# Kernel optimization log

Hardware: AMD Instinct MI355X
Metric: run time of the kernel (lower is better)

## Reference

```python
import jax, jax.numpy as jnp
import numpy as np

B, S, E, D = 4, 2048, 1024, 1024
NEG_INF = float('-inf')


def setup_inputs() -> dict:
    key = jax.random.key(0)
    ks = jax.random.split(key, 10)
    query = jax.random.normal(ks[0], (B, S, E), dtype=jnp.float32)
    key_t = jax.random.normal(ks[1], (B, S, E), dtype=jnp.float32)
    value = jax.random.normal(ks[2], (B, S, E), dtype=jnp.float32)
    # Linear params (torch convention: y = x @ W.T + b)
    sc = 1.0 / np.sqrt(E)
    Wq = jax.random.uniform(ks[3], (D, E), jnp.float32, -sc, sc)
    bq = jax.random.uniform(ks[4], (D,), jnp.float32, -sc, sc)
    Wk = jax.random.uniform(ks[5], (D, E), jnp.float32, -sc, sc)
    bk = jax.random.uniform(ks[6], (D,), jnp.float32, -sc, sc)
    Wv = jax.random.uniform(ks[7], (D, E), jnp.float32, -sc, sc)
    bv = jax.random.uniform(ks[8], (D,), jnp.float32, -sc, sc)
    # padding mask: True = masked key position; ensure key 0 is never masked
    # so no row is fully -inf under the causal mask.
    lengths = jax.random.randint(ks[9], (B, 1, 1), 1, S + 1)  # valid length per batch
    pos = jnp.arange(S)[None, None, :]
    padding_mask = pos >= lengths  # [B,1,S] bool
    return {
        "query": query, "key": key_t, "value": value,
        "Wq": Wq, "bq": bq, "Wk": Wk, "bk": bk, "Wv": Wv, "bv": bv,
        "padding_mask": padding_mask, "look_ahead_mask": 1,
    }


def reference(query, key, value, Wq, bq, Wk, bk, Wv, bv, padding_mask, look_ahead_mask):
    q = query @ Wq.T + bq          # [B,S,D]
    k = key @ Wk.T + bk            # [B,S,D]
    v = value @ Wv.T + bv          # [B,S,D]
    scale = jnp.sqrt(jnp.asarray(q.shape[-1], q.dtype))
    qk = jnp.einsum('bqd,bkd->bqk', q, k) / scale  # [B,S,S]
    if padding_mask is not None:
        qk = jnp.where(padding_mask, NEG_INF, qk)
    if look_ahead_mask:
        causal = jnp.where(
            jnp.tril(jnp.ones((q.shape[1], k.shape[1]), dtype=bool)),
            jnp.asarray(0.0, qk.dtype), jnp.asarray(NEG_INF, qk.dtype))
        qk = qk + causal
    attn = jax.nn.softmax(qk, axis=-1)
    return jnp.einsum('bqk,bkd->bqd', attn, v)  # [B,S,D]
```

## Files before the change

kernel.cpp:

```cpp
#include <hip/hip_runtime.h>
#include <cstdint>
#include <cstddef>

#define B_ 4
#define S_ 2048
#define E_ 1024
#define D_ 1024
#define MFLAT (B_*S_)

typedef __attribute__((ext_vector_type(4))) float f32x4;
typedef __attribute__((ext_vector_type(8))) short short8;
typedef unsigned short u16;
typedef unsigned int   u32;

__device__ __forceinline__ u16 f2bf(float f) {
  u32 u = __float_as_uint(f);
  u = (u + 0x7fffu + ((u >> 16) & 1u)) >> 16;
  return (u16)u;
}

__device__ __forceinline__ void gll16(const void* g, void* lds) {
  __builtin_amdgcn_global_load_lds(
      (const __attribute__((address_space(1))) void*)g,
      (__attribute__((address_space(3))) void*)lds, 16, 0, 0);
}

__device__ __forceinline__ void gemm_core(
    const u16* __restrict__ Ag, int lda,
    const u16* __restrict__ Bg, int ldb,
    int ksteps, u16* As, u16* Bs, f32x4 acc[4][4])
{
  const int tid = threadIdx.x;
  const int w = tid >> 6;
  const int l = tid & 63;
  const int srow = l >> 2;
  const int skb  = (l & 3) << 3;
  const int fr = l & 15;
  const int fk = (l >> 4) << 3;
  const int wr = (w >> 1) << 6;
  const int wc = (w & 1) << 6;
  const int c0 = w * 2, c1 = c0 + 1;

  const u16* a0 = Ag + (size_t)(c0*16 + srow)*lda + skb;
  const u16* a1 = Ag + (size_t)(c1*16 + srow)*lda + skb;
  const u16* b0 = Bg + (size_t)(c0*16 + srow)*ldb + skb;
  const u16* b1 = Bg + (size_t)(c1*16 + srow)*ldb + skb;

  for (int kt = 0; kt < ksteps; ++kt) {
    gll16(a0, As + c0*512);
    gll16(a1, As + c1*512);
    gll16(b0, Bs + c0*512);
    gll16(b1, Bs + c1*512);
    a0 += 32; a1 += 32; b0 += 32; b1 += 32;
    __syncthreads();
    short8 af[4], bfr[4];
#pragma unroll
    for (int i = 0; i < 4; ++i)
      af[i] = *(const short8*)(As + ((wr + i*16 + fr) << 5) + fk);
#pragma unroll
    for (int j = 0; j < 4; ++j)
      bfr[j] = *(const short8*)(Bs + ((wc + j*16 + fr) << 5) + fk);
#pragma unroll
    for (int i = 0; i < 4; ++i)
#pragma unroll
      for (int j = 0; j < 4; ++j)
        acc[i][j] = __builtin_amdgcn_mfma_f32_16x16x32_bf16(af[i], bfr[j], acc[i][j], 0, 0, 0);
    __syncthreads();
  }
}

__global__ __launch_bounds__(256) void cvt_kernel(const float* __restrict__ src,
                                                  u16* __restrict__ dst, int n4) {
  int idx = blockIdx.x * blockDim.x + threadIdx.x;
  int stride = gridDim.x * blockDim.x;
  for (int i = idx; i < n4; i += stride) {
    float4 f = ((const float4*)src)[i];
    ushort4 o;
    o.x = f2bf(f.x); o.y = f2bf(f.y); o.z = f2bf(f.z); o.w = f2bf(f.w);
    ((ushort4*)dst)[i] = o;
  }
}

__global__ __launch_bounds__(256) void lengths_kernel(const void* __restrict__ mask,
                                                      int* __restrict__ lengths) {
  __shared__ int isbytes;
  const int t = threadIdx.x;
  if (t == 0) isbytes = 0;
  __syncthreads();
  const int* wi = (const int*)mask;
  int bad = 0;
  for (int idx = t; idx < (B_*S_)/4; idx += 256) {
    int v = wi[idx];
    if (v != 0 && v != 1) bad = 1;
  }
  if (bad) atomicOr(&isbytes, 1);
  __syncthreads();
  const int isb = isbytes;
  const int w = t >> 6, l = t & 63;
  const unsigned char* mb = (const unsigned char*)mask;
  int cnt = 0;
  for (int j = l; j < S_; j += 64) {
    int val = isb ? (int)mb[(size_t)w*S_ + j] : wi[(size_t)w*S_ + j];
    cnt += (val == 0);
  }
#pragma unroll
  for (int off = 32; off >= 1; off >>= 1) cnt += __shfl_xor(cnt, off);
  if (l == 0) lengths[w] = cnt;
}

__global__ __launch_bounds__(256) void proj_kernel(
    const u16* __restrict__ X, const u16* __restrict__ W,
    const float* __restrict__ bq, const float* __restrict__ bk, const float* __restrict__ bv,
    u16* __restrict__ q, u16* __restrict__ k, u16* __restrict__ v)
{
  __shared__ u16 As[4096], Bs[4096];
  const int nt = blockIdx.x, mt = blockIdx.y, z = blockIdx.z;
  const u16* Xz = X + (size_t)z * ((size_t)MFLAT * E_);
  const u16* Wz = W + (size_t)z * ((size_t)D_ * E_);
  f32x4 acc[4][4];
#pragma unroll
  for (int i = 0; i < 4; ++i)
#pragma unroll
    for (int j = 0; j < 4; ++j) acc[i][j] = (f32x4){0.f,0.f,0.f,0.f};
  gemm_core(Xz + (size_t)(mt*128)*E_, E_, Wz + (size_t)(nt*128)*E_, E_, E_/32, As, Bs, acc);

  const float* bias = (z == 0) ? bq : (z == 1) ? bk : bv;
  u16* out = (z == 0) ? q : (z == 1) ? k : v;
  const int tid = threadIdx.x, w = tid >> 6, l = tid & 63;
  const int wr = (w >> 1) << 6, wc = (w & 1) << 6;
  const int orow = mt*128 + wr + ((l >> 4) << 2);
  const int ocol = nt*128 + wc + (l & 15);
#pragma unroll
  for (int i = 0; i < 4; ++i)
#pragma unroll
    for (int j = 0; j < 4; ++j) {
      const int col = ocol + j*16;
      const float bcol = bias[col];
#pragma unroll
      for (int r = 0; r < 4; ++r) {
        const int row = orow + i*16 + r;
        out[(size_t)row*D_ + col] = f2bf(acc[i][j][r] + bcol);
      }
    }
}

__global__ __launch_bounds__(256) void transpose_kernel(
    const u16* __restrict__ v, u16* __restrict__ vT)
{
  __shared__ u16 tl[64][68];
  const int xt = blockIdx.x;
  const int yt = blockIdx.y;
  const int b  = blockIdx.z;
  const int t = threadIdx.x;
  const int r0 = t >> 4;
  const int c4 = (t & 15) << 2;
  const u16* src = v + ((size_t)b*S_ + yt*64)*D_ + xt*64;
#pragma unroll
  for (int rr = r0; rr < 64; rr += 16) {
    ushort4 u = *(const ushort4*)(src + (size_t)rr*D_ + c4);
    tl[rr][c4+0] = u.x; tl[rr][c4+1] = u.y; tl[rr][c4+2] = u.z; tl[rr][c4+3] = u.w;
  }
  __syncthreads();
  u16* dst = vT + ((size_t)b*D_ + xt*64)*S_ + yt*64;
#pragma unroll
  for (int rr = r0; rr < 64; rr += 16) {
    ushort4 u;
    u.x = tl[c4+0][rr]; u.y = tl[c4+1][rr]; u.z = tl[c4+2][rr]; u.w = tl[c4+3][rr];
    *(ushort4*)(dst + (size_t)rr*S_ + c4) = u;
  }
}

__global__ __launch_bounds__(256) void qk_kernel(
    const u16* __restrict__ q, const u16* __restrict__ k,
    const int* __restrict__ lengths, float* __restrict__ scores)
{
  const int tx = blockIdx.x, ty = blockIdx.y, b = blockIdx.z;
  if (tx > ty) return;
  const int len = lengths[b];
  if (tx * 128 >= len) return;
  __shared__ u16 As[4096], Bs[4096];
  f32x4 acc[4][4];
#pragma unroll
  for (int i = 0; i < 4; ++i)
#pragma unroll
    for (int j = 0; j < 4; ++j) acc[i][j] = (f32x4){0.f,0.f,0.f,0.f};
  const u16* Aq = q + ((size_t)b*S_ + (size_t)ty*128) * D_;
  const u16* Bk = k + ((size_t)b*S_ + (size_t)tx*128) * D_;
  gemm_core(Aq, D_, Bk, D_, D_/32, As, Bs, acc);

  const int tid = threadIdx.x, w = tid >> 6, l = tid & 63;
  const int wr = (w >> 1) << 6, wc = (w & 1) << 6;
  const int orow = ty*128 + wr + ((l >> 4) << 2);
  const int ocol = tx*128 + wc + (l & 15);
  float* sb = scores + (size_t)b*S_*S_;
#pragma unroll
  for (int i = 0; i < 4; ++i)
#pragma unroll
    for (int j = 0; j < 4; ++j)
#pragma unroll
      for (int r = 0; r < 4; ++r)
        sb[(size_t)(orow + i*16 + r)*S_ + (ocol + j*16)] = acc[i][j][r] * 0.03125f;
}

__global__ __launch_bounds__(256) void softmax_kernel(
    const float* __restrict__ scores, const int* __restrict__ lengths,
    u16* __restrict__ P)
{
  const int i = blockIdx.x, b = blockIdx.y;
  const int len = lengths[b];
  const int kmax = min(i + 1, len);
  const float* row = scores + ((size_t)b*S_ + i)*S_;
  u16* prow = P + ((size_t)b*S_ + i)*S_;
  const int t = threadIdx.x;
  const int j0 = t * 8;
  float v[8];
  {
    float4 x0 = *(const float4*)(row + j0);
    float4 x1 = *(const float4*)(row + j0 + 4);
    v[0]=x0.x; v[1]=x0.y; v[2]=x0.z; v[3]=x0.w;
    v[4]=x1.x; v[5]=x1.y; v[6]=x1.z; v[7]=x1.w;
  }
  float m = -3.4e38f;
#pragma unroll
  for (int e = 0; e < 8; ++e) if (j0 + e < kmax) m = fmaxf(m, v[e]);
#pragma unroll
  for (int off = 32; off >= 1; off >>= 1) m = fmaxf(m, __shfl_xor(m, off));
  __shared__ float redm[4], reds[4];
  if ((t & 63) == 0) redm[t >> 6] = m;
  __syncthreads();
  m = fmaxf(fmaxf(redm[0], redm[1]), fmaxf(redm[2], redm[3]));
  float s = 0.f, ex[8];
#pragma unroll
  for (int e = 0; e < 8; ++e) {
    ex[e] = (j0 + e < kmax) ? __expf(v[e] - m) : 0.f;
    s += ex[e];
  }
#pragma unroll
  for (int off = 32; off >= 1; off >>= 1) s += __shfl_xor(s, off);
  if ((t & 63) == 0) reds[t >> 6] = s;
  __syncthreads();
  s = reds[0] + reds[1] + reds[2] + reds[3];
  const float inv = 1.0f / s;
  short8 o;
#pragma unroll
  for (int e = 0; e < 8; ++e) o[e] = (short)f2bf(ex[e] * inv);
  *(short8*)(prow + j0) = o;
}

__global__ __launch_bounds__(256) void pv_kernel(
    const u16* __restrict__ P, const u16* __restrict__ vT,
    const int* __restrict__ lengths, float* __restrict__ out)
{
  const int xt = blockIdx.x, ty = blockIdx.y, b = blockIdx.z;
  const int len = lengths[b];
  const int kend = min(ty*128 + 128, len);
  const int ksteps = (kend + 31) >> 5;
  __shared__ u16 As[4096], Bs[4096];
  f32x4 acc[4][4];
#pragma unroll
  for (int i = 0; i < 4; ++i)
#pragma unroll
    for (int j = 0; j < 4; ++j) acc[i][j] = (f32x4){0.f,0.f,0.f,0.f};
  const u16* Ap = P  + ((size_t)b*S_ + (size_t)ty*128)*S_;
  const u16* Bv = vT + ((size_t)b*D_ + (size_t)xt*128)*S_;
  gemm_core(Ap, S_, Bv, S_, ksteps, As, Bs, acc);

  const int tid = threadIdx.x, w = tid >> 6, l = tid & 63;
  const int wr = (w >> 1) << 6, wc = (w & 1) << 6;
  const int orow = ty*128 + wr + ((l >> 4) << 2);
  const int ocol = xt*128 + wc + (l & 15);
  float* ob = out + (size_t)b*S_*D_;
#pragma unroll
  for (int i = 0; i < 4; ++i)
#pragma unroll
    for (int j = 0; j < 4; ++j)
#pragma unroll
      for (int r = 0; r < 4; ++r)
        ob[(size_t)(orow + i*16 + r)*D_ + (ocol + j*16)] = acc[i][j][r];
}

extern "C" void kernel_launch(void* const* d_in, const int* in_sizes, int n_in,
                              void* d_out, int out_size, void* d_ws, size_t ws_size,
                              hipStream_t stream)
{
  const float* query = (const float*)d_in[0];
  const float* key_  = (const float*)d_in[1];
  const float* value = (const float*)d_in[2];
  const float* Wq = (const float*)d_in[3];
  const float* bq = (const float*)d_in[4];
  const float* Wk = (const float*)d_in[5];
  const float* bk = (const float*)d_in[6];
  const float* Wv = (const float*)d_in[7];
  const float* bv = (const float*)d_in[8];
  const void*  pmask = d_in[9];
  float* out = (float*)d_out;
  char* ws = (char*)d_ws;

  int* lengths = (int*)ws;
  u16* q   = (u16*)(ws + 256);
  u16* kk  = q  + (size_t)MFLAT * D_;
  u16* vT  = kk + (size_t)MFLAT * D_;
  u16* Pbuf = (u16*)(ws + 50331904ull);
  u16* vbuf = Pbuf;
  char* scratch = ws + 83886336ull;
  u16* Xb = (u16*)scratch;
  u16* Wb = Xb + 3ull * MFLAT * E_;
  float* scores = (float*)scratch;

  cvt_kernel<<<dim3(2048), 256, 0, stream>>>(query, Xb,                 (MFLAT*E_)/4);
  cvt_kernel<<<dim3(2048), 256, 0, stream>>>(key_,  Xb + (size_t)MFLAT*E_,   (MFLAT*E_)/4);
  cvt_kernel<<<dim3(2048), 256, 0, stream>>>(value, Xb + 2ull*MFLAT*E_, (MFLAT*E_)/4);
  cvt_kernel<<<dim3(256),  256, 0, stream>>>(Wq, Wb,                    (D_*E_)/4);
  cvt_kernel<<<dim3(256),  256, 0, stream>>>(Wk, Wb + (size_t)D_*E_,    (D_*E_)/4);
  cvt_kernel<<<dim3(256),  256, 0, stream>>>(Wv, Wb + 2ull*D_*E_,       (D_*E_)/4);
  lengths_kernel<<<dim3(1), 256, 0, stream>>>(pmask, lengths);

  proj_kernel<<<dim3(8, 64, 3), 256, 0, stream>>>(Xb, Wb, bq, bk, bv, q, kk, vbuf);

  transpose_kernel<<<dim3(16, 32, 4), 256, 0, stream>>>(vbuf, vT);

  qk_kernel<<<dim3(16, 16, 4), 256, 0, stream>>>(q, kk, lengths, scores);

  softmax_kernel<<<dim3(2048, 4), 256, 0, stream>>>(scores, lengths, Pbuf);

  pv_kernel<<<dim3(8, 16, 4), 256, 0, stream>>>(Pbuf, vT, lengths, out);
}
```

Before: 379.2 us.

## Use 256x256 tiled, double-buffered 8-wave GEMM core for projection and QK

Adds a new GEMM core that computes 256x256 output tiles with 512 threads, a K step of 64, XOR-swizzled LDS, double-buffered global-to-LDS loads staged in quarters interleaved with MFMA work, and priority hints around MFMA. The projection and QK score kernels switch to this core and launch fewer, larger blocks with 128 KB dynamic LDS. This is meant to raise arithmetic intensity and hide load latency in the two large GEMMs. Larger tiles make the causal and padding tile skipping in QK coarser, and the high LDS and register use limits occupancy.

```diff
diff --git a/kernel.cpp b/kernel.cpp
--- a/kernel.cpp
+++ b/kernel.cpp
@@ -23,6 +23,135 @@
   __builtin_amdgcn_global_load_lds(
       (const __attribute__((address_space(1))) void*)g,
       (__attribute__((address_space(3))) void*)lds, 16, 0, 0);
+}
+
+#define BARRIER() do { asm volatile("" ::: "memory"); \
+                       __builtin_amdgcn_s_barrier();  \
+                       asm volatile("" ::: "memory"); } while (0)
+
+__device__ __forceinline__ void gemm256_core(
+    const u16* __restrict__ Ag, int lda,
+    const u16* __restrict__ Bg, int ldb,
+    int NT, char* lds, f32x4 acc[8][4])
+{
+  const int tid = threadIdx.x;
+  const int w  = tid >> 6;
+  const int l  = tid & 63;
+  const int wm = w >> 2;
+  const int wn = w & 3;
+
+  const int srow = tid >> 3;
+  const int scs  = ((tid & 7) << 4) ^ ((srow & 7) << 4);
+
+  const int fr = l & 15;
+  const int kq = l >> 4;
+  const int kcol0 = (kq << 4) ^ ((l & 7) << 4);
+  const int kcol1 = ((kq << 4) + 64) ^ ((l & 7) << 4);
+  const int aoff = wm * 16384 + fr * 128;
+  const int boff = 65536 + (wn >> 1) * 16384 + (((wn & 1) * 64 + fr) * 128);
+
+  const int nhalf = 4 * NT;
+
+#define STAGE_HALF(h_) do {                                                        \
+    const int h__ = (h_);                                                          \
+    if (h__ < nhalf) {                                                             \
+      const int T__ = h__ >> 2, r__ = h__ & 3, buf__ = T__ & 1;                    \
+      const char* s0; char* d0; size_t rstep;                                      \
+      if (r__ < 2) {                                                               \
+        s0 = (const char*)Bg + ((((size_t)(r__*128 + srow)) * (size_t)ldb          \
+                                 + (size_t)T__*64) << 1) + scs;                    \
+        d0 = lds + 65536 + buf__*32768 + r__*16384 + (w << 10);                    \
+        rstep = ((size_t)ldb) << 7;                                                \
+      } else {                                                                     \
+        s0 = (const char*)Ag + ((((size_t)((r__-2)*128 + srow)) * (size_t)lda      \
+                                 + (size_t)T__*64) << 1) + scs;                    \
+        d0 = lds + buf__*32768 + (r__-2)*16384 + (w << 10);                        \
+        rstep = ((size_t)lda) << 7;                                                \
+      }                                                                            \
+      gll16(s0, d0);                                                               \
+      gll16(s0 + rstep, d0 + 8192);                                                \
+    }                                                                              \
+  } while (0)
+
+#define LDA_F(mf, kc) (*(const short8*)(lds + bufo + aoff + (mf)*2048 + (kc)))
+#define LDB_F(nf, kc) (*(const short8*)(lds + bufo + boff + (nf)*2048 + (kc)))
+
+#define WAIT_LGKM() do { asm volatile("s_waitcnt lgkmcnt(0)" ::: "memory"); \
+                         __builtin_amdgcn_sched_barrier(0); } while (0)
+
+#define MFMA_Q(jbase) do {                                                         \
+    __builtin_amdgcn_s_setprio(1);                                                 \
+    _Pragma("unroll")                                                              \
+    for (int i = 0; i < 4; ++i) {                                                  \
+      _Pragma("unroll")                                                            \
+      for (int j = 0; j < 2; ++j) {                                                \
+        acc[accm + i][(jbase) + j] = __builtin_amdgcn_mfma_f32_16x16x32_bf16(      \
+            areg[i][0], breg[(jbase)+j][0], acc[accm + i][(jbase)+j], 0, 0, 0);    \
+        acc[accm + i][(jbase) + j] = __builtin_amdgcn_mfma_f32_16x16x32_bf16(      \
+            areg[i][1], breg[(jbase)+j][1], acc[accm + i][(jbase)+j], 0, 0, 0);    \
+      }                                                                            \
+    }                                                                              \
+    __builtin_amdgcn_s_setprio(0);                                                 \
+  } while (0)
+
+  short8 areg[4][2], breg[4][2];
+
+  STAGE_HALF(0); STAGE_HALF(1); STAGE_HALF(2); STAGE_HALF(3);
+  STAGE_HALF(4); STAGE_HALF(5);
+  asm volatile("s_waitcnt vmcnt(4)" ::: "memory");
+  BARRIER();
+
+  for (int t = 0; t < NT; ++t) {
+    const int bufo = (t & 1) << 15;
+    const int hb = 4 * t + 6;
+
+    {
+      int accm = 0;
+#pragma unroll
+      for (int i = 0; i < 4; ++i) { areg[i][0] = LDA_F(i, kcol0); areg[i][1] = LDA_F(i, kcol1); }
+#pragma unroll
+      for (int j = 0; j < 2; ++j) { breg[j][0] = LDB_F(j, kcol0); breg[j][1] = LDB_F(j, kcol1); }
+      STAGE_HALF(hb + 0);
+      BARRIER();
+      WAIT_LGKM();
+      MFMA_Q(0);
+      BARRIER();
+    }
+    {
+      int accm = 0;
+#pragma unroll
+      for (int j = 2; j < 4; ++j) { breg[j][0] = LDB_F(j, kcol0); breg[j][1] = LDB_F(j, kcol1); }
+      STAGE_HALF(hb + 1);
+      BARRIER();
+      WAIT_LGKM();
+      MFMA_Q(2);
+      BARRIER();
+    }
+    {
+      int accm = 4;
+#pragma unroll
+      for (int i = 0; i < 4; ++i) { areg[i][0] = LDA_F(4 + i, kcol0); areg[i][1] = LDA_F(4 + i, kcol1); }
+      STAGE_HALF(hb + 2);
+      BARRIER();
+      WAIT_LGKM();
+      MFMA_Q(0);
+      BARRIER();
+    }
+    {
+      int accm = 4;
+      STAGE_HALF(hb + 3);
+      BARRIER();
+      WAIT_LGKM();
+      MFMA_Q(2);
+      asm volatile("s_waitcnt vmcnt(4)" ::: "memory");
+      BARRIER();
+    }
+  }
+#undef STAGE_HALF
+#undef LDA_F
+#undef LDB_F
+#undef WAIT_LGKM
+#undef MFMA_Q
 }
 
 __device__ __forceinline__ void gemm_core(
@@ -108,40 +237,40 @@
   if (l == 0) lengths[w] = cnt;
 }
 
-__global__ __launch_bounds__(256) void proj_kernel(
+__global__ __launch_bounds__(512, 2) void proj256_kernel(
     const u16* __restrict__ X, const u16* __restrict__ W,
     const float* __restrict__ bq, const float* __restrict__ bk, const float* __restrict__ bv,
     u16* __restrict__ q, u16* __restrict__ k, u16* __restrict__ v)
 {
-  __shared__ u16 As[4096], Bs[4096];
+  extern __shared__ char lds[];
   const int nt = blockIdx.x, mt = blockIdx.y, z = blockIdx.z;
-  const u16* Xz = X + (size_t)z * ((size_t)MFLAT * E_);
-  const u16* Wz = W + (size_t)z * ((size_t)D_ * E_);
-  f32x4 acc[4][4];
-#pragma unroll
-  for (int i = 0; i < 4; ++i)
+  const u16* Xz = X + (size_t)z * ((size_t)MFLAT * E_) + (size_t)(mt*256)*E_;
+  const u16* Wz = W + (size_t)z * ((size_t)D_ * E_)    + (size_t)(nt*256)*E_;
+  f32x4 acc[8][4];
+#pragma unroll
+  for (int i = 0; i < 8; ++i)
 #pragma unroll
     for (int j = 0; j < 4; ++j) acc[i][j] = (f32x4){0.f,0.f,0.f,0.f};
-  gemm_core(Xz + (size_t)(mt*128)*E_, E_, Wz + (size_t)(nt*128)*E_, E_, E_/32, As, Bs, acc);
+
+  gemm256_core(Xz, E_, Wz, E_, E_/64, lds, acc);
 
   const float* bias = (z == 0) ? bq : (z == 1) ? bk : bv;
   u16* out = (z == 0) ? q : (z == 1) ? k : v;
   const int tid = threadIdx.x, w = tid >> 6, l = tid & 63;
-  const int wr = (w >> 1) << 6, wc = (w & 1) << 6;
-  const int orow = mt*128 + wr + ((l >> 4) << 2);
-  const int ocol = nt*128 + wc + (l & 15);
-#pragma unroll
-  for (int i = 0; i < 4; ++i)
-#pragma unroll
-    for (int j = 0; j < 4; ++j) {
-      const int col = ocol + j*16;
-      const float bcol = bias[col];
-#pragma unroll
-      for (int r = 0; r < 4; ++r) {
-        const int row = orow + i*16 + r;
-        out[(size_t)row*D_ + col] = f2bf(acc[i][j][r] + bcol);
-      }
-    }
+  const int wm = w >> 2, wn = w & 3;
+  const int fr = l & 15, kq = l >> 4;
+  const int orow0 = mt*256 + wm*128 + kq*4;
+  const int ocol0 = nt*256 + wn*64 + fr;
+#pragma unroll
+  for (int nf = 0; nf < 4; ++nf) {
+    const int col = ocol0 + nf*16;
+    const float bcol = bias[col];
+#pragma unroll
+    for (int mf = 0; mf < 8; ++mf)
+#pragma unroll
+      for (int r = 0; r < 4; ++r)
+        out[(size_t)(orow0 + mf*16 + r)*D_ + col] = f2bf(acc[mf][nf][r] + bcol);
+  }
 }
 
 __global__ __launch_bounds__(256) void transpose_kernel(
@@ -170,36 +299,37 @@
   }
 }
 
-__global__ __launch_bounds__(256) void qk_kernel(
+__global__ __launch_bounds__(512, 2) void qk256_kernel(
     const u16* __restrict__ q, const u16* __restrict__ k,
     const int* __restrict__ lengths, float* __restrict__ scores)
 {
   const int tx = blockIdx.x, ty = blockIdx.y, b = blockIdx.z;
   if (tx > ty) return;
   const int len = lengths[b];
-  if (tx * 128 >= len) return;
-  __shared__ u16 As[4096], Bs[4096];
-  f32x4 acc[4][4];
-#pragma unroll
-  for (int i = 0; i < 4; ++i)
+  if (tx * 256 >= len) return;
+  extern __shared__ char lds[];
+  f32x4 acc[8][4];
+#pragma unroll
+  for (int i = 0; i < 8; ++i)
 #pragma unroll
     for (int j = 0; j < 4; ++j) acc[i][j] = (f32x4){0.f,0.f,0.f,0.f};
-  const u16* Aq = q + ((size_t)b*S_ + (size_t)ty*128) * D_;
-  const u16* Bk = k + ((size_t)b*S_ + (size_t)tx*128) * D_;
-  gemm_core(Aq, D_, Bk, D_, D_/32, As, Bs, acc);
+  const u16* Aq = q + ((size_t)b*S_ + (size_t)ty*256) * D_;
+  const u16* Bk = k + ((size_t)b*S_ + (size_t)tx*256) * D_;
+  gemm256_core(Aq, D_, Bk, D_, D_/64, lds, acc);
 
   const int tid = threadIdx.x, w = tid >> 6, l = tid & 63;
-  const int wr = (w >> 1) << 6, wc = (w & 1) << 6;
-  const int orow = ty*128 + wr + ((l >> 4) << 2);
-  const int ocol = tx*128 + wc + (l & 15);
+  const int wm = w >> 2, wn = w & 3;
+  const int fr = l & 15, kq = l >> 4;
+  const int orow0 = ty*256 + wm*128 + kq*4;
+  const int ocol0 = tx*256 + wn*64 + fr;
   float* sb = scores + (size_t)b*S_*S_;
 #pragma unroll
-  for (int i = 0; i < 4; ++i)
-#pragma unroll
-    for (int j = 0; j < 4; ++j)
+  for (int mf = 0; mf < 8; ++mf)
+#pragma unroll
+    for (int nf = 0; nf < 4; ++nf)
 #pragma unroll
       for (int r = 0; r < 4; ++r)
-        sb[(size_t)(orow + i*16 + r)*S_ + (ocol + j*16)] = acc[i][j][r] * 0.03125f;
+        sb[(size_t)(orow0 + mf*16 + r)*S_ + (ocol0 + nf*16)] = acc[mf][nf][r] * 0.03125f;
 }
 
 __global__ __launch_bounds__(256) void softmax_kernel(
@@ -296,6 +426,11 @@
   float* out = (float*)d_out;
   char* ws = (char*)d_ws;
 
+  (void)hipFuncSetAttribute((const void*)proj256_kernel,
+                            hipFuncAttributeMaxDynamicSharedMemorySize, 131072);
+  (void)hipFuncSetAttribute((const void*)qk256_kernel,
+                            hipFuncAttributeMaxDynamicSharedMemorySize, 131072);
+
   int* lengths = (int*)ws;
   u16* q   = (u16*)(ws + 256);
   u16* kk  = q  + (size_t)MFLAT * D_;
@@ -315,11 +450,11 @@
   cvt_kernel<<<dim3(256),  256, 0, stream>>>(Wv, Wb + 2ull*D_*E_,       (D_*E_)/4);
   lengths_kernel<<<dim3(1), 256, 0, stream>>>(pmask, lengths);
 
-  proj_kernel<<<dim3(8, 64, 3), 256, 0, stream>>>(Xb, Wb, bq, bk, bv, q, kk, vbuf);
+  proj256_kernel<<<dim3(4, 32, 3), 512, 131072, stream>>>(Xb, Wb, bq, bk, bv, q, kk, vbuf);
 
   transpose_kernel<<<dim3(16, 32, 4), 256, 0, stream>>>(vbuf, vT);
 
-  qk_kernel<<<dim3(16, 16, 4), 256, 0, stream>>>(q, kk, lengths, scores);
+  qk256_kernel<<<dim3(8, 8, 4), 512, 131072, stream>>>(q, kk, lengths, scores);
 
   softmax_kernel<<<dim3(2048, 4), 256, 0, stream>>>(scores, lengths, Pbuf);
 
```

Result: no change. 373.2 us (-1.6%).
